# Kernel optimization log

Hardware: AMD Instinct MI355X
Metric: run time of the kernel (lower is better)

## Reference

```python
import jax, jax.numpy as jnp
import numpy as np

HINGE_VALUE = 1.0

def setup_inputs() -> dict:
    key = jax.random.key(0)
    k1, k2 = jax.random.split(key)
    x_pred = jax.random.normal(k1, (8192, 128), dtype=jnp.float32)
    x_target = jax.random.normal(k2, (16384, 128), dtype=jnp.float32)
    return {"x_pred": x_pred, "x_target": x_target, "top_k": 5}


def _cdist(a, b):
    # Euclidean distance via GEMM form: ||a||^2 + ||b||^2 - 2 a.b
    a2 = jnp.sum(a * a, axis=-1, keepdims=True)          # [N,1]
    b2 = jnp.sum(b * b, axis=-1, keepdims=True).T        # [1,M]
    d2 = a2 + b2 - 2.0 * (a @ b.T)                       # [N,M]
    return jnp.sqrt(jnp.maximum(d2, 0.0))


def reference(x_pred, x_target, top_k):
    c_dist = _cdist(x_pred, x_target)                    # [N,M]
    # smallest-k distances per pred point
    neg_vals, _ = jax.lax.top_k(-c_dist, top_k)          # [N,k]
    values = jnp.maximum(-neg_vals - HINGE_VALUE, 0.0)   # hinge
    return jnp.mean(values)
```

## Files before the change

### kernel.cpp

```cpp
#include <hip/hip_runtime.h>
#include <hip/hip_bf16.h>
#include <float.h>

#define N_PRED 8192
#define M_TGT  16384
#define KD     128
#define TOPK   5
#define SPLITS 16
#define MSPLIT (M_TGT / SPLITS)
#define TILE_T 128
#define NTILES (MSPLIT / TILE_T)
#define ROWS_PER_BLOCK 256
#define ROWBLKS (N_PRED / ROWS_PER_BLOCK)
#define NBLKROW (SPLITS * 16)
#define FIN_BLOCKS 512

using short8  = __attribute__((ext_vector_type(8))) short;
using floatx4 = __attribute__((ext_vector_type(4))) float;

__device__ __forceinline__ unsigned short f2bf(float v) {
    unsigned int u = __float_as_uint(v);
    u = (u + 0x7FFFu + ((u >> 16) & 1u)) >> 16;
    return (unsigned short)u;
}

__device__ __forceinline__ void async16(const void* g, void* l) {
    __builtin_amdgcn_global_load_lds(
        (const __attribute__((address_space(1))) unsigned int*)g,
        (__attribute__((address_space(3))) unsigned int*)l, 16, 0, 0);
}
__device__ __forceinline__ void async4(const void* g, void* l) {
    __builtin_amdgcn_global_load_lds(
        (const __attribute__((address_space(1))) unsigned int*)g,
        (__attribute__((address_space(3))) unsigned int*)l, 4, 0, 0);
}

__device__ __forceinline__ void ins5(float* t, float d) {
    t[4] = __builtin_amdgcn_fmed3f(d, t[3], t[4]);
    t[3] = __builtin_amdgcn_fmed3f(d, t[2], t[3]);
    t[2] = __builtin_amdgcn_fmed3f(d, t[1], t[2]);
    t[1] = __builtin_amdgcn_fmed3f(d, t[0], t[1]);
    t[0] = fminf(t[0], d);
}

__device__ __forceinline__ void bmerge(float* u) {
    #pragma unroll
    for (int off = 1; off < 64; off <<= 1) {
        float o0 = __shfl_xor(u[0], off);
        float o1 = __shfl_xor(u[1], off);
        float o2 = __shfl_xor(u[2], off);
        float o3 = __shfl_xor(u[3], off);
        float o4 = __shfl_xor(u[4], off);
        ins5(u, o0); ins5(u, o1); ins5(u, o2); ins5(u, o3); ins5(u, o4);
    }
}

__device__ __forceinline__ float dotd(unsigned int p, unsigned int t) {
    const float plo = __uint_as_float(p << 16);
    const float phi = __uint_as_float(p & 0xFFFF0000u);
    const float tlo = __uint_as_float(t << 16);
    const float thi = __uint_as_float(t & 0xFFFF0000u);
    return plo * tlo + phi * thi;
}

__global__ void prep_kernel(const float* __restrict__ pred,
                            const float* __restrict__ tgt,
                            unsigned short* __restrict__ predB,
                            unsigned short* __restrict__ tgtB,
                            float* __restrict__ a2,
                            float* __restrict__ b2,
                            float* __restrict__ acc,
                            unsigned int* __restrict__ counter) {
    const int row = blockIdx.x * 8 + (threadIdx.x >> 5);
    const int l32 = threadIdx.x & 31;
    const float* src;
    unsigned short* dst;
    float scale;
    float* norm;
    if (row < N_PRED) {
        src = pred + (size_t)row * KD;
        dst = predB + (size_t)row * KD;
        scale = -2.0f;
        norm = a2 + row;
    } else {
        const int rr = row - N_PRED;
        src = tgt + (size_t)rr * KD;
        dst = tgtB + (size_t)rr * KD;
        scale = 1.0f;
        norm = b2 + rr;
    }
    const float4 x = reinterpret_cast<const float4*>(src)[l32];
    uint2 p;
    p.x = (unsigned int)f2bf(x.x * scale) | ((unsigned int)f2bf(x.y * scale) << 16);
    p.y = (unsigned int)f2bf(x.z * scale) | ((unsigned int)f2bf(x.w * scale) << 16);
    reinterpret_cast<uint2*>(dst)[l32] = p;
    float s = x.x * x.x + x.y * x.y + x.z * x.z + x.w * x.w;
    #pragma unroll
    for (int off = 16; off > 0; off >>= 1) s += __shfl_down(s, off, 32);
    if (l32 == 0) norm[0] = s;
    if (blockIdx.x == 0 && threadIdx.x == 0) { acc[0] = 0.0f; counter[0] = 0u; }
}

__global__ __launch_bounds__(512, 4) void density_kernel(
        const unsigned short* __restrict__ predB,
        const unsigned short* __restrict__ tgtB,
        const float* __restrict__ b2,
        float2* __restrict__ wsMin) {
    const int tid   = threadIdx.x;
    const int wave  = tid >> 6;
    const int lane  = tid & 63;
    const int col   = lane & 15;
    const int quad  = lane >> 4;
    const int split = blockIdx.x & (SPLITS - 1);
    const int rowblk = blockIdx.x >> 4;
    const int r0 = rowblk * ROWS_PER_BLOCK + wave * 32;
    const int m0 = split * MSPLIT;

    __shared__ short8 frag[2][TILE_T * 16];
    __shared__ float  b2s[2][TILE_T];

    short8 afrag[2][4];
    #pragma unroll
    for (int rf = 0; rf < 2; rf++)
        #pragma unroll
        for (int kf = 0; kf < 4; kf++)
            afrag[rf][kf] = *reinterpret_cast<const short8*>(
                predB + (size_t)(r0 + rf * 16 + col) * KD + kf * 32 + quad * 8);

    float2 bm[2][4];
    #pragma unroll
    for (int rf = 0; rf < 2; rf++)
        #pragma unroll
        for (int rg = 0; rg < 4; rg++)
            bm[rf][rg] = make_float2(FLT_MAX, FLT_MAX);

    {
        #pragma unroll
        for (int s = 0; s < 4; ++s) {
            const int ci = wave * 4 + s, g = ci >> 2, kf = ci & 3;
            const unsigned short* src =
                tgtB + (size_t)(m0 + g * 16 + col) * KD + kf * 32 + quad * 8;
            async16(src, &frag[0][ci * 64]);
        }
        if (wave < 2) async4(b2 + m0 + wave * 64 + lane, &b2s[0][wave * 64]);
    }
    __syncthreads();

    for (int t = 0; t < NTILES; ++t) {
        const int cur = t & 1;
        if (t + 1 < NTILES) {
            const int m0t = m0 + (t + 1) * TILE_T;
            #pragma unroll
            for (int s = 0; s < 4; ++s) {
                const int ci = wave * 4 + s, g = ci >> 2, kf = ci & 3;
                const unsigned short* src =
                    tgtB + (size_t)(m0t + g * 16 + col) * KD + kf * 32 + quad * 8;
                async16(src, &frag[cur ^ 1][ci * 64]);
            }
            if (wave < 2) async4(b2 + m0t + wave * 64 + lane, &b2s[cur ^ 1][wave * 64]);
        }

        #pragma unroll
        for (int g = 0; g < 8; ++g) {
            const float bq = b2s[cur][g * 16 + col];
            short8 bf[4];
            #pragma unroll
            for (int kf = 0; kf < 4; ++kf)
                bf[kf] = frag[cur][(g * 4 + kf) * 64 + lane];
            const floatx4 ci = {bq, bq, bq, bq};
            #pragma unroll
            for (int rf = 0; rf < 2; ++rf) {
                floatx4 c;
                c = __builtin_amdgcn_mfma_f32_16x16x32_bf16(afrag[rf][0], bf[0], ci, 0, 0, 0);
                c = __builtin_amdgcn_mfma_f32_16x16x32_bf16(afrag[rf][1], bf[1], c, 0, 0, 0);
                c = __builtin_amdgcn_mfma_f32_16x16x32_bf16(afrag[rf][2], bf[2], c, 0, 0, 0);
                c = __builtin_amdgcn_mfma_f32_16x16x32_bf16(afrag[rf][3], bf[3], c, 0, 0, 0);
                #pragma unroll
                for (int rg = 0; rg < 4; ++rg) {
                    const float d = c[rg];
                    bm[rf][rg].y = __builtin_amdgcn_fmed3f(d, bm[rf][rg].x, bm[rf][rg].y);
                    bm[rf][rg].x = fminf(bm[rf][rg].x, d);
                }
            }
        }
        __syncthreads();
    }

    #pragma unroll
    for (int rf = 0; rf < 2; ++rf)
        #pragma unroll
        for (int rg = 0; rg < 4; ++rg) {
            const int row = r0 + rf * 16 + quad * 4 + rg;
            wsMin[((size_t)row * SPLITS + split) * 16 + col] = bm[rf][rg];
        }
}

__global__ __launch_bounds__(512) void finalize_kernel(
        const float2* __restrict__ wsMin,
        const unsigned short* __restrict__ predB,
        const unsigned short* __restrict__ tgtB,
        const float* __restrict__ b2,
        const float* __restrict__ a2,
        float* __restrict__ acc,
        unsigned int* __restrict__ counter,
        float* __restrict__ out) {
    const int wave = threadIdx.x >> 6;
    const int lane = threadIdx.x & 63;

    float wsum = 0.0f;
    #pragma unroll 1
    for (int i = 0; i < 2; ++i) {
        const int row = (blockIdx.x * 8 + wave) * 2 + i;

        const float2* pv = wsMin + (size_t)row * NBLKROW + lane * 4;
        float2 v[4];
        #pragma unroll
        for (int j = 0; j < 4; ++j) v[j] = pv[j];

        float u[5] = {FLT_MAX, FLT_MAX, FLT_MAX, FLT_MAX, FLT_MAX};
        #pragma unroll
        for (int j = 0; j < 4; ++j) { ins5(u, v[j].x); ins5(u, v[j].y); }
        bmerge(u);
        const float m5 = u[4];

        unsigned long long fl[4];
        #pragma unroll
        for (int j = 0; j < 4; ++j) fl[j] = __ballot(v[j].y <= m5);

        if (fl[0] | fl[1] | fl[2] | fl[3]) {
            #pragma unroll
            for (int j = 0; j < 4; ++j)
                if (v[j].y <= m5) { v[j].x = FLT_MAX; v[j].y = FLT_MAX; }
            #pragma unroll
            for (int j = 0; j < 5; ++j) u[j] = FLT_MAX;
            #pragma unroll
            for (int j = 0; j < 4; ++j) { ins5(u, v[j].x); ins5(u, v[j].y); }
            bmerge(u);
            #pragma unroll
            for (int j = 0; j < 4; ++j) {
                unsigned long long m = fl[j];
                while (m) {
                    const int bit = __ffsll((unsigned long long)m) - 1;
                    m &= m - 1;
                    const int blk = bit * 4 + j;
                    const int sp = blk >> 4, cb = blk & 15;
                    const int tg = sp * MSPLIT + lane * 16 + cb;
                    float s = b2[tg];
                    const uint4* tp = reinterpret_cast<const uint4*>(tgtB + (size_t)tg * KD);
                    const uint4* pp = reinterpret_cast<const uint4*>(predB + (size_t)row * KD);
                    #pragma unroll
                    for (int q = 0; q < 16; ++q) {
                        const uint4 pa = pp[q], tb = tp[q];
                        s += dotd(pa.x, tb.x) + dotd(pa.y, tb.y)
                           + dotd(pa.z, tb.z) + dotd(pa.w, tb.w);
                    }
                    float w[5] = {s, FLT_MAX, FLT_MAX, FLT_MAX, FLT_MAX};
                    bmerge(w);
                    #pragma unroll
                    for (int q = 0; q < 5; ++q) ins5(u, w[q]);
                }
            }
        }

        const float a = a2[row];
        #pragma unroll
        for (int j = 0; j < 5; ++j) {
            const float dd = sqrtf(fmaxf(u[j] + a, 0.0f));
            wsum += fmaxf(dd - 1.0f, 0.0f);
        }
    }

    __shared__ float hsum[8];
    if (lane == 0) hsum[wave] = wsum;
    __syncthreads();
    if (threadIdx.x == 0) {
        float tot = 0.0f;
        #pragma unroll
        for (int w = 0; w < 8; ++w) tot += hsum[w];
        atomicAdd(acc, tot);
        const unsigned int done = atomicAdd(counter, 1u);
        if (done == gridDim.x - 1) {
            const float t = atomicAdd(acc, 0.0f);
            out[0] = t * (1.0f / (float)(N_PRED * TOPK));
        }
    }
}

extern "C" void kernel_launch(void* const* d_in, const int* in_sizes, int n_in,
                              void* d_out, int out_size, void* d_ws, size_t ws_size,
                              hipStream_t stream) {
    const float* pred = (const float*)d_in[0];
    const float* tgt  = (const float*)d_in[1];
    char* ws = (char*)d_ws;
    unsigned short* predB = (unsigned short*)(ws);
    unsigned short* tgtB  = (unsigned short*)(ws + (size_t)2 * 1024 * 1024);
    float* a2     = (float*)(ws + (size_t)6 * 1024 * 1024);
    float* b2     = (float*)(ws + (size_t)6 * 1024 * 1024 + 32 * 1024);
    float* acc    = (float*)(ws + (size_t)6 * 1024 * 1024 + 96 * 1024);
    unsigned int* counter = (unsigned int*)(ws + (size_t)6 * 1024 * 1024 + 96 * 1024 + 64);
    float2* wsMin = (float2*)(ws + (size_t)6 * 1024 * 1024 + 128 * 1024);
    float* out = (float*)d_out;

    prep_kernel<<<(N_PRED + M_TGT) / 8, 256, 0, stream>>>(pred, tgt, predB, tgtB, a2, b2, acc, counter);
    density_kernel<<<ROWBLKS * SPLITS, 512, 0, stream>>>(predB, tgtB, b2, wsMin);
    finalize_kernel<<<FIN_BLOCKS, 512, 0, stream>>>(wsMin, predB, tgtB, b2, a2, acc, counter, out);
}
```

Measured before the change: 125.6 us.

## Pre-reduce per-column min pairs across lanes before writing workspace

The GEMM kernel now merges its per-lane best-two distance pairs across groups of four columns with xor shuffles, so it writes 4 pairs per row per split instead of 16. This shrinks the workspace traffic and lets the finalize kernel read one float2 per lane instead of four. The exchange is that each flagged bucket now stands for 4 target columns, so the finalize fallback must recompute 4 dot products per flagged bucket rather than 1. That adds refinement work whenever a bucket's second-best value is within the top-5 threshold.

```diff
diff --git a/kernel.cpp b/kernel.cpp
--- a/kernel.cpp
+++ b/kernel.cpp
@@ -12,7 +12,7 @@
 #define NTILES (MSPLIT / TILE_T)
 #define ROWS_PER_BLOCK 256
 #define ROWBLKS (N_PRED / ROWS_PER_BLOCK)
-#define NBLKROW (SPLITS * 16)
+#define NBLKROW (SPLITS * 4)
 #define FIN_BLOCKS 512
 
 using short8  = __attribute__((ext_vector_type(8))) short;
@@ -190,8 +190,19 @@
     for (int rf = 0; rf < 2; ++rf)
         #pragma unroll
         for (int rg = 0; rg < 4; ++rg) {
-            const int row = r0 + rf * 16 + quad * 4 + rg;
-            wsMin[((size_t)row * SPLITS + split) * 16 + col] = bm[rf][rg];
+            float t1 = bm[rf][rg].x, t2 = bm[rf][rg].y;
+            #pragma unroll
+            for (int off = 8; off >= 4; off >>= 1) {
+                const float o1 = __shfl_xor(t1, off);
+                const float o2 = __shfl_xor(t2, off);
+                const float n1 = fminf(t1, o1);
+                const float n2 = fminf(fmaxf(t1, o1), fminf(t2, o2));
+                t1 = n1; t2 = n2;
+            }
+            if (col < 4) {
+                const int row = r0 + rf * 16 + quad * 4 + rg;
+                wsMin[(size_t)row * NBLKROW + split * 4 + col] = make_float2(t1, t2);
+            }
         }
 }
 
@@ -212,53 +223,44 @@
     for (int i = 0; i < 2; ++i) {
         const int row = (blockIdx.x * 8 + wave) * 2 + i;
 
-        const float2* pv = wsMin + (size_t)row * NBLKROW + lane * 4;
-        float2 v[4];
-        #pragma unroll
-        for (int j = 0; j < 4; ++j) v[j] = pv[j];
+        float2 v = wsMin[(size_t)row * NBLKROW + lane];
 
         float u[5] = {FLT_MAX, FLT_MAX, FLT_MAX, FLT_MAX, FLT_MAX};
-        #pragma unroll
-        for (int j = 0; j < 4; ++j) { ins5(u, v[j].x); ins5(u, v[j].y); }
+        ins5(u, v.x); ins5(u, v.y);
         bmerge(u);
         const float m5 = u[4];
 
-        unsigned long long fl[4];
-        #pragma unroll
-        for (int j = 0; j < 4; ++j) fl[j] = __ballot(v[j].y <= m5);
-
-        if (fl[0] | fl[1] | fl[2] | fl[3]) {
-            #pragma unroll
-            for (int j = 0; j < 4; ++j)
-                if (v[j].y <= m5) { v[j].x = FLT_MAX; v[j].y = FLT_MAX; }
+        unsigned long long fl = __ballot(v.y <= m5);
+
+        if (fl) {
+            if (v.y <= m5) { v.x = FLT_MAX; v.y = FLT_MAX; }
             #pragma unroll
             for (int j = 0; j < 5; ++j) u[j] = FLT_MAX;
-            #pragma unroll
-            for (int j = 0; j < 4; ++j) { ins5(u, v[j].x); ins5(u, v[j].y); }
+            ins5(u, v.x); ins5(u, v.y);
             bmerge(u);
-            #pragma unroll
-            for (int j = 0; j < 4; ++j) {
-                unsigned long long m = fl[j];
-                while (m) {
-                    const int bit = __ffsll((unsigned long long)m) - 1;
-                    m &= m - 1;
-                    const int blk = bit * 4 + j;
-                    const int sp = blk >> 4, cb = blk & 15;
-                    const int tg = sp * MSPLIT + lane * 16 + cb;
+            unsigned long long m = fl;
+            while (m) {
+                const int blk = __ffsll((unsigned long long)m) - 1;
+                m &= m - 1;
+                const int sp = blk >> 2, cg = blk & 3;
+                const uint4* pp = reinterpret_cast<const uint4*>(predB + (size_t)row * KD);
+                float w[5] = {FLT_MAX, FLT_MAX, FLT_MAX, FLT_MAX, FLT_MAX};
+                #pragma unroll
+                for (int h = 0; h < 4; ++h) {
+                    const int tg = sp * MSPLIT + lane * 16 + cg + 4 * h;
                     float s = b2[tg];
                     const uint4* tp = reinterpret_cast<const uint4*>(tgtB + (size_t)tg * KD);
-                    const uint4* pp = reinterpret_cast<const uint4*>(predB + (size_t)row * KD);
                     #pragma unroll
                     for (int q = 0; q < 16; ++q) {
                         const uint4 pa = pp[q], tb = tp[q];
                         s += dotd(pa.x, tb.x) + dotd(pa.y, tb.y)
                            + dotd(pa.z, tb.z) + dotd(pa.w, tb.w);
                     }
-                    float w[5] = {s, FLT_MAX, FLT_MAX, FLT_MAX, FLT_MAX};
-                    bmerge(w);
-                    #pragma unroll
-                    for (int q = 0; q < 5; ++q) ins5(u, w[q]);
+                    ins5(w, s);
                 }
+                bmerge(w);
+                #pragma unroll
+                for (int q = 0; q < 5; ++q) ins5(u, w[q]);
             }
         }
 
```

New measurement: 144.4 us. 1.15x slower.
